# Kernel tuning notes

Hardware: AMD Instinct MI355X
Metric: run time of the kernel (lower is better)

Reference implementation:

```python
import jax, jax.numpy as jnp
import numpy as np

NUM_HEADS = 8
NUM_KV_HEADS = 4
HEAD_DIM = 256
HIDDEN = 2048
SEQ = 4096
CHUNK_START = 2048
CHUNK_END = 4096
SOFTCAP = 50.0
EPS = 1e-6
ROPE_THETA = 10000.0
NEG_INF = -1e9


def _rms_norm(x, w, eps=EPS):
    # Gemma RMSNorm: computed in fp32, scale is (1 + w)
    x32 = x.astype(jnp.float32)
    out = x32 * jax.lax.rsqrt(jnp.mean(x32 * x32, axis=-1, keepdims=True) + eps)
    return (out * (1.0 + w.astype(jnp.float32))).astype(x.dtype)


def _rotate_half(x):
    h = x.shape[-1] // 2
    return jnp.concatenate([-x[..., h:], x[..., :h]], axis=-1)


def _apply_rope(x, cos, sin):
    # x: [B, S, H, D]; cos/sin: [B, S, D] -> unsqueeze head dim
    cos = cos[:, :, None, :]
    sin = sin[:, :, None, :]
    return x * cos + _rotate_half(x) * sin


def setup_inputs() -> dict:
    key = jax.random.key(0)
    ks = jax.random.split(key, 8)
    hidden_states = jax.random.normal(ks[0], (1, SEQ, HIDDEN), dtype=jnp.float32)
    # real RoPE tables
    inv_freq = 1.0 / (ROPE_THETA ** (np.arange(0, HEAD_DIM, 2, dtype=np.float32) / HEAD_DIM))
    pos = np.arange(SEQ, dtype=np.float32)
    freqs = np.outer(pos, inv_freq)                      # [S, D/2]
    emb = np.concatenate([freqs, freqs], axis=-1)        # [S, D]
    cos = jnp.asarray(np.cos(emb))[None]                 # [1, S, D]
    sin = jnp.asarray(np.sin(emb))[None]
    # causal additive mask for the chunk: query i (abs pos start+i) attends keys j <= start+i
    q_pos = np.arange(CHUNK_START, CHUNK_END)[:, None]
    k_pos = np.arange(CHUNK_END)[None, :]
    attention_mask = jnp.asarray(np.where(k_pos <= q_pos, 0.0, NEG_INF).astype(np.float32))[None, None]
    s = 0.02
    wq = jax.random.normal(ks[1], (HIDDEN, NUM_HEADS * HEAD_DIM), dtype=jnp.float32) * s
    wk = jax.random.normal(ks[2], (HIDDEN, NUM_KV_HEADS * HEAD_DIM), dtype=jnp.float32) * s
    wv = jax.random.normal(ks[3], (HIDDEN, NUM_KV_HEADS * HEAD_DIM), dtype=jnp.float32) * s
    wo = jax.random.normal(ks[4], (NUM_HEADS * HEAD_DIM, HIDDEN), dtype=jnp.float32) * s
    q_norm_w = jnp.zeros((HEAD_DIM,), dtype=jnp.float32)
    k_norm_w = jnp.zeros((HEAD_DIM,), dtype=jnp.float32)
    v_norm_w = jnp.zeros((HEAD_DIM,), dtype=jnp.float32)
    return {
        'hidden_states': hidden_states, 'cos': cos, 'sin': sin,
        'attention_mask': attention_mask,
        'wq': wq, 'wk': wk, 'wv': wv, 'wo': wo,
        'q_norm_w': q_norm_w, 'k_norm_w': k_norm_w, 'v_norm_w': v_norm_w,
        'start': CHUNK_START, 'end': CHUNK_END,
    }


def reference(hidden_states, cos, sin, attention_mask, wq, wk, wv, wo,
              q_norm_w, k_norm_w, v_norm_w, start, end):
    B = hidden_states.shape[0]
    chunk = end - start
    scaling = HEAD_DIM ** -0.5

    # ---- queries from the chunk ----
    q = (hidden_states[:, start:end] @ wq).reshape(B, chunk, NUM_HEADS, HEAD_DIM)
    q = _rms_norm(q, q_norm_w)
    q = _apply_rope(q, cos[:, start:end], sin[:, start:end])
    q = q.transpose(0, 2, 1, 3)                         # [B, H, chunk, D]

    # ---- keys / values over [0, end) ----
    kv_h = hidden_states[:, :end]
    k = (kv_h @ wk).reshape(B, end, NUM_KV_HEADS, HEAD_DIM)
    k = _rms_norm(k, k_norm_w)
    k = _apply_rope(k, cos[:, :end], sin[:, :end]).transpose(0, 2, 1, 3)   # [B, KV, end, D]
    v = (kv_h @ wv).reshape(B, end, NUM_KV_HEADS, HEAD_DIM)
    v = _rms_norm(v, v_norm_w).transpose(0, 2, 1, 3)                        # [B, KV, end, D]

    # ---- GQA repeat_kv ----
    n_rep = NUM_HEADS // NUM_KV_HEADS
    k = jnp.repeat(k, n_rep, axis=1)                    # [B, H, end, D]
    v = jnp.repeat(v, n_rep, axis=1)

    # ---- eager attention with logit softcap ----
    logits = jnp.einsum('bhqd,bhkd->bhqk', q, k) * scaling
    logits = jnp.tanh(logits / SOFTCAP) * SOFTCAP
    logits = logits + attention_mask
    attn = jax.nn.softmax(logits.astype(jnp.float32), axis=-1).astype(q.dtype)
    out = jnp.einsum('bhqk,bhkd->bhqd', attn, v)
    out = out.transpose(0, 2, 1, 3).reshape(B, chunk, NUM_HEADS * HEAD_DIM)
    return out @ wo
```

## Files before the change

kernel.cpp:

```cpp
#include <hip/hip_runtime.h>

#define HID 2048
#define SEQL 4096
#define CHUNK 2048
#define NHEADS 8
#define NKVH 4
#define HDIM 256

typedef __bf16 bf16x4 __attribute__((ext_vector_type(4)));
typedef __bf16 bf16x8 __attribute__((ext_vector_type(8)));
typedef float f32x4 __attribute__((ext_vector_type(4)));
typedef _Float16 f16x4 __attribute__((ext_vector_type(4)));
typedef __attribute__((address_space(1))) unsigned int* as1_u32;
typedef __attribute__((address_space(3))) unsigned int* as3_u32;

__device__ __forceinline__ void load_lds16(const __bf16* g, __bf16* l) {
  __builtin_amdgcn_global_load_lds((as1_u32)g, (as3_u32)l, 16, 0, 0);
}

__global__ void cvt_bf16_kernel(const float* __restrict__ X, __bf16* __restrict__ Y) {
  int i = blockIdx.x * blockDim.x + threadIdx.x;
  const float4* xv = (const float4*)X;
  float4 v = xv[i];
  bf16x4 o;
  o[0] = (__bf16)v.x; o[1] = (__bf16)v.y; o[2] = (__bf16)v.z; o[3] = (__bf16)v.w;
  *(bf16x4*)(Y + i * 4) = o;
}

__global__ void transpose_all_kernel(const float* __restrict__ wq, const float* __restrict__ wk,
                                     const float* __restrict__ wv, const float* __restrict__ wo,
                                     __bf16* __restrict__ WQT, __bf16* __restrict__ WKVT,
                                     __bf16* __restrict__ WOT) {
  __shared__ float tile[64][65];
  const int b = blockIdx.x;
  const float* W;
  __bf16* WT;
  int R, C, bx, by;
  if (b < 1024) { W = wq; WT = WQT; R = 2048; C = 2048; bx = b & 31; by = b >> 5; }
  else if (b < 1536) { int q = b - 1024; W = wk; WT = WKVT; R = 2048; C = 1024; bx = q & 15; by = q >> 4; }
  else if (b < 2048) { int q = b - 1536; W = wv; WT = WKVT + (size_t)1024 * 2048; R = 2048; C = 1024; bx = q & 15; by = q >> 4; }
  else { int q = b - 2048; W = wo; WT = WOT; R = 2048; C = 2048; bx = q & 31; by = q >> 5; }
  int r0 = by * 64, c0 = bx * 64;
  for (int i = threadIdx.x; i < 4096; i += 256) {
    int r = i >> 6, c = i & 63;
    tile[r][c] = W[(size_t)(r0 + r) * C + c0 + c];
  }
  __syncthreads();
  for (int i = threadIdx.x; i < 4096; i += 256) {
    int c = i >> 6, r = i & 63;
    WT[(size_t)(c0 + c) * R + r0 + r] = (__bf16)tile[r][c];
  }
}

__global__ __launch_bounds__(256, 3) void proj_kernel(
    const __bf16* __restrict__ Xb, const __bf16* __restrict__ WQT,
    const __bf16* __restrict__ WKVT, __bf16* __restrict__ Qp, __bf16* __restrict__ KVp) {
  __shared__ __bf16 Asm[128 * 32];
  __shared__ __bf16 Bsm[128 * 32];
  const int tid = threadIdx.x;
  const int lane = tid & 63, wave = tid >> 6;
  const int quad = lane >> 4, l15 = lane & 15;
  const int b = blockIdx.x;
  const __bf16 *A, *B;
  __bf16* C;
  int m0, n0;
  if (b < 512) {
    A = Xb; B = WKVT; C = KVp;
    m0 = (b & 31) * 128; n0 = (b >> 5) * 128;
  } else {
    int q = b - 512;
    A = Xb + (size_t)2048 * 2048; B = WQT; C = Qp;
    m0 = (q & 15) * 128; n0 = (q >> 4) * 128;
  }
  const int wm = (wave & 1) * 64, wn = (wave >> 1) * 64;
  f32x4 acc[4][4];
#pragma unroll
  for (int i = 0; i < 4; i++)
#pragma unroll
    for (int j = 0; j < 4; j++) acc[i][j] = (f32x4){0.f, 0.f, 0.f, 0.f};

  const int rA = lane >> 2, cA = (lane & 3) * 8;

  for (int k0 = 0; k0 < 2048; k0 += 32) {
#pragma unroll
    for (int c = wave; c < 8; c += 4) {
      load_lds16(A + (size_t)(m0 + c * 16 + rA) * 2048 + k0 + cA, Asm + c * 512);
      load_lds16(B + (size_t)(n0 + c * 16 + rA) * 2048 + k0 + cA, Bsm + c * 512);
    }
    __syncthreads();
    bf16x8 af[4], bfr[4];
#pragma unroll
    for (int i = 0; i < 4; i++) {
      af[i] = *(const bf16x8*)(Asm + (wm + i * 16 + l15) * 32 + quad * 8);
      bfr[i] = *(const bf16x8*)(Bsm + (wn + i * 16 + l15) * 32 + quad * 8);
    }
#pragma unroll
    for (int mi = 0; mi < 4; mi++)
#pragma unroll
      for (int ni = 0; ni < 4; ni++)
        acc[mi][ni] = __builtin_amdgcn_mfma_f32_16x16x32_bf16(af[mi], bfr[ni], acc[mi][ni], 0, 0, 0);
    __syncthreads();
  }
#pragma unroll
  for (int mi = 0; mi < 4; mi++) {
    int r = m0 + wm + mi * 16 + quad * 4;
#pragma unroll
    for (int ni = 0; ni < 4; ni++) {
      int cc = n0 + wn + ni * 16 + l15;
#pragma unroll
      for (int j = 0; j < 4; j++)
        C[(size_t)(r + j) * 2048 + cc] = (__bf16)acc[mi][ni][j];
    }
  }
}

template <int NI, bool F32OUT>
__global__ __launch_bounds__(256, 2) void gemm_bt_kernel(
    const __bf16* __restrict__ A, const __bf16* __restrict__ B,
    void* __restrict__ Cv, int M, int N, int Kd) {
  constexpr int BN = NI * 32;
  __shared__ __bf16 Asm[128 * 32];
  __shared__ __bf16 Bsm[BN * 32];
  const int tid = threadIdx.x;
  const int lane = tid & 63, wave = tid >> 6;
  const int quad = lane >> 4, l15 = lane & 15;
  const int m0 = blockIdx.x * 128, n0 = blockIdx.y * BN;
  const int wm = (wave & 1) * 64, wn = (wave >> 1) * (NI * 16);
  f32x4 acc[4][NI];
#pragma unroll
  for (int i = 0; i < 4; i++)
#pragma unroll
    for (int j = 0; j < NI; j++) acc[i][j] = (f32x4){0.f, 0.f, 0.f, 0.f};

  const int rA = lane >> 2, cA = (lane & 3) * 8;

  for (int k0 = 0; k0 < Kd; k0 += 32) {
#pragma unroll
    for (int c = wave; c < 8; c += 4)
      load_lds16(A + (size_t)(m0 + c * 16 + rA) * Kd + k0 + cA, Asm + c * 512);
#pragma unroll
    for (int c = wave; c < BN / 16; c += 4)
      load_lds16(B + (size_t)(n0 + c * 16 + rA) * Kd + k0 + cA, Bsm + c * 512);
    __syncthreads();
    bf16x8 af[4], bfr[NI];
#pragma unroll
    for (int i = 0; i < 4; i++)
      af[i] = *(const bf16x8*)(Asm + (wm + i * 16 + l15) * 32 + quad * 8);
#pragma unroll
    for (int i = 0; i < NI; i++)
      bfr[i] = *(const bf16x8*)(Bsm + (wn + i * 16 + l15) * 32 + quad * 8);
#pragma unroll
    for (int mi = 0; mi < 4; mi++)
#pragma unroll
      for (int ni = 0; ni < NI; ni++)
        acc[mi][ni] = __builtin_amdgcn_mfma_f32_16x16x32_bf16(af[mi], bfr[ni], acc[mi][ni], 0, 0, 0);
    __syncthreads();
  }
#pragma unroll
  for (int mi = 0; mi < 4; mi++) {
    int r = m0 + wm + mi * 16 + quad * 4;
#pragma unroll
    for (int ni = 0; ni < NI; ni++) {
      int cc = n0 + wn + ni * 16 + l15;
#pragma unroll
      for (int j = 0; j < 4; j++) {
        if (F32OUT)
          ((float*)Cv)[(size_t)(r + j) * N + cc] = acc[mi][ni][j];
        else
          ((__bf16*)Cv)[(size_t)(r + j) * N + cc] = (__bf16)acc[mi][ni][j];
      }
    }
  }
}

__global__ void norm_all_kernel(__bf16* __restrict__ Qp, __bf16* __restrict__ KVp,
                                __bf16* __restrict__ VT,
                                const float* __restrict__ cosb, const float* __restrict__ sinb,
                                const float* __restrict__ qw, const float* __restrict__ kw,
                                const float* __restrict__ vw) {
  const int gw = (blockIdx.x * 256 + threadIdx.x) >> 6;
  const int lane = threadIdx.x & 63;
  const int d0 = lane * 4;

  __bf16* row;
  const float* w;
  int pos = -1;
  int vh = 0, vt = 0;
  bool isV = false;
  float prescale = 1.f;
  if (gw < 16384) {
    int t = gw >> 3, h = gw & 7;
    row = Qp + (size_t)t * 2048 + h * 256;
    w = qw; pos = t + 2048; prescale = 0.0625f;
  } else {
    int g2 = gw - 16384;
    int t = g2 >> 3, r = g2 & 7;
    if (r < 4) {
      row = KVp + (size_t)t * 2048 + r * 256;
      w = kw; pos = t;
    } else {
      row = KVp + (size_t)t * 2048 + 1024 + (r - 4) * 256;
      w = vw; isV = true; vh = r - 4; vt = t;
    }
  }

  bf16x4 rv = *(const bf16x4*)(row + d0);
  float x[4];
  float ss = 0.f;
#pragma unroll
  for (int j = 0; j < 4; j++) { x[j] = (float)rv[j]; ss += x[j] * x[j]; }
#pragma unroll
  for (int off = 1; off < 64; off <<= 1) ss += __shfl_xor(ss, off);
  float scale = rsqrtf(ss * (1.f / 256.f) + 1e-6f);
  float n[4];
#pragma unroll
  for (int j = 0; j < 4; j++) n[j] = x[j] * scale * (1.f + w[d0 + j]);

  if (!isV) {
    const float* cp = cosb + (size_t)pos * 256 + d0;
    const float* sp = sinb + (size_t)pos * 256 + d0;
    bf16x4 ov;
#pragma unroll
    for (int j = 0; j < 4; j++) {
      float other = __shfl_xor(n[j], 32);
      float rot = (lane < 32) ? -other : other;
      ov[j] = (__bf16)((n[j] * cp[j] + rot * sp[j]) * prescale);
    }
    *(bf16x4*)(row + d0) = ov;
  } else {
#pragma unroll
    for (int j = 0; j < 4; j++)
      VT[(size_t)vh * (256 * 4096) + (size_t)(d0 + j) * 4096 + vt] = (__bf16)n[j];
  }
}

__global__ __launch_bounds__(256, 2) void attn_kernel(
    const __bf16* __restrict__ Q,
    const __bf16* __restrict__ K,
    const __bf16* __restrict__ VT,
    _Float16* __restrict__ Op,
    float* __restrict__ Lp) {
  __shared__ __bf16 Ksm[2][8][32][32];
  __shared__ __bf16 Vsm[2][256][32];
  __shared__ __bf16 Pex[4][32][40];
  const int tid = threadIdx.x;
  const int lane = tid & 63, wave = tid >> 6;
  const int quad = lane >> 4, l15 = lane & 15;
  const int b = blockIdx.x;
  const int idx = b & 255;
  const int h = idx & 7, sp = (idx >> 3) & 3;
  int qt = idx >> 5;
  if (b >= 256) qt = 15 - qt;
  const int kvh = h >> 1;

  const int T = 68 + 4 * qt;
  const int nst = T >> 2;

  bf16x8 qf[2][8];
#pragma unroll
  for (int r = 0; r < 2; r++) {
    const __bf16* qp = Q + (size_t)(qt * 128 + wave * 32 + r * 16 + l15) * 2048 + h * 256 + quad * 8;
#pragma unroll
    for (int s = 0; s < 8; s++) qf[r][s] = *(const bf16x8*)(qp + s * 32);
  }
  f32x4 o[2][16];
#pragma unroll
  for (int r = 0; r < 2; r++)
#pragma unroll
    for (int i = 0; i < 16; i++) o[r][i] = (f32x4){0.f, 0.f, 0.f, 0.f};
  float rs[2][4] = {{0.f, 0.f, 0.f, 0.f}, {0.f, 0.f, 0.f, 0.f}};

  const __bf16* Kb = K + kvh * 256;
  const __bf16* Vb = VT + (size_t)kvh * (256 * 4096);
  const int rA = lane >> 2;
  const int cAs = (((lane & 3) ^ ((rA >> 1) & 3)) * 8);
  const int kx = (quad ^ ((l15 >> 1) & 3)) * 8;
  const int qbase = 2048 + qt * 128 + wave * 32 + quad * 4;

  {
    const int t0 = sp * 32;
#pragma unroll
    for (int ch = 0; ch < 4; ch++) {
      int cc = wave + ch * 4;
      int s = cc >> 1, hf = cc & 1;
      load_lds16(Kb + (size_t)(t0 + hf * 16 + rA) * 2048 + s * 32 + cAs, &Ksm[0][s][hf * 16][0]);
      load_lds16(Vb + (size_t)(cc * 16 + rA) * 4096 + t0 + cAs, &Vsm[0][cc * 16][0]);
    }
  }

  for (int i = 0; i < nst; i++) {
    const int buf = i & 1;
    const int t0 = (4 * i + sp) * 32;
    __syncthreads();
    if (i + 1 < nst) {
      const int t1 = t0 + 128;
#pragma unroll
      for (int ch = 0; ch < 4; ch++) {
        int cc = wave + ch * 4;
        int s = cc >> 1, hf = cc & 1;
        load_lds16(Kb + (size_t)(t1 + hf * 16 + rA) * 2048 + s * 32 + cAs, &Ksm[buf ^ 1][s][hf * 16][0]);
        load_lds16(Vb + (size_t)(cc * 16 + rA) * 4096 + t1 + cAs, &Vsm[buf ^ 1][cc * 16][0]);
      }
    }

    f32x4 s4[2][2];
    s4[0][0] = (f32x4){0.f, 0.f, 0.f, 0.f};
    s4[0][1] = s4[0][0]; s4[1][0] = s4[0][0]; s4[1][1] = s4[0][0];
    __builtin_amdgcn_s_setprio(1);
#pragma unroll
    for (int s = 0; s < 8; s++) {
      bf16x8 b0 = *(const bf16x8*)(&Ksm[buf][s][l15][kx]);
      bf16x8 b1 = *(const bf16x8*)(&Ksm[buf][s][16 + l15][kx]);
      s4[0][0] = __builtin_amdgcn_mfma_f32_16x16x32_bf16(qf[0][s], b0, s4[0][0], 0, 0, 0);
      s4[0][1] = __builtin_amdgcn_mfma_f32_16x16x32_bf16(qf[0][s], b1, s4[0][1], 0, 0, 0);
      s4[1][0] = __builtin_amdgcn_mfma_f32_16x16x32_bf16(qf[1][s], b0, s4[1][0], 0, 0, 0);
      s4[1][1] = __builtin_amdgcn_mfma_f32_16x16x32_bf16(qf[1][s], b1, s4[1][1], 0, 0, 0);
    }
    __builtin_amdgcn_s_setprio(0);

    const bool mk = (i == nst - 1);
#pragma unroll
    for (int r = 0; r < 2; r++)
#pragma unroll
      for (int nt = 0; nt < 2; nt++) {
        const int key = t0 + nt * 16 + l15;
#pragma unroll
        for (int j = 0; j < 4; j++) {
          float v = s4[r][nt][j];
          float e = __expf(v * 0.04f);
          float p = __expf(-100.f * __builtin_amdgcn_rcpf(e + 1.f));
          if (mk && key > qbase + r * 16 + j) p = 0.f;
          s4[r][nt][j] = p;
          rs[r][j] += p;
        }
      }

#pragma unroll
    for (int r = 0; r < 2; r++)
#pragma unroll
      for (int nt = 0; nt < 2; nt++)
#pragma unroll
        for (int j = 0; j < 4; j++)
          Pex[wave][r * 16 + quad * 4 + j][nt * 16 + l15] = (__bf16)s4[r][nt][j];

    bf16x8 pf0 = *(const bf16x8*)(&Pex[wave][l15][quad * 8]);
    bf16x8 pf1 = *(const bf16x8*)(&Pex[wave][16 + l15][quad * 8]);
    __builtin_amdgcn_s_setprio(1);
#pragma unroll
    for (int d = 0; d < 16; d++) {
      bf16x8 vf = *(const bf16x8*)(&Vsm[buf][d * 16 + l15][kx]);
      o[0][d] = __builtin_amdgcn_mfma_f32_16x16x32_bf16(pf0, vf, o[0][d], 0, 0, 0);
      o[1][d] = __builtin_amdgcn_mfma_f32_16x16x32_bf16(pf1, vf, o[1][d], 0, 0, 0);
    }
    __builtin_amdgcn_s_setprio(0);
  }

#pragma unroll
  for (int off = 1; off < 16; off <<= 1)
#pragma unroll
    for (int r = 0; r < 2; r++)
#pragma unroll
      for (int j = 0; j < 4; j++) rs[r][j] += __shfl_xor(rs[r][j], off);

  _Float16* Os = Op + (size_t)sp * (2048 * 2048);
  float* Ls = Lp + sp * (2048 * 8);
#pragma unroll
  for (int r = 0; r < 2; r++) {
    float inv[4];
#pragma unroll
    for (int j = 0; j < 4; j++)
      inv[j] = rs[r][j] > 0.f ? 1.f / rs[r][j] : 0.f;
    const int trow = qt * 128 + wave * 32 + r * 16 + quad * 4;
#pragma unroll
    for (int d = 0; d < 16; d++) {
      const int col = h * 256 + d * 16 + l15;
#pragma unroll
      for (int j = 0; j < 4; j++)
        Os[(size_t)(trow + j) * 2048 + col] = (_Float16)(o[r][d][j] * inv[j]);
    }
    if (l15 == 0) {
#pragma unroll
      for (int j = 0; j < 4; j++) Ls[(trow + j) * 8 + h] = rs[r][j];
    }
  }
}

__global__ void merge_kernel(const _Float16* __restrict__ Op, const float* __restrict__ Lp,
                             __bf16* __restrict__ AO) {
  int f = (blockIdx.x * 256 + threadIdx.x) * 4;
  int q = f >> 11, col = f & 2047, h = col >> 8;
  float lsum = 0.f;
  float acc[4] = {0.f, 0.f, 0.f, 0.f};
#pragma unroll
  for (int s = 0; s < 4; s++) {
    float l = Lp[s * (2048 * 8) + q * 8 + h];
    lsum += l;
    f16x4 v = *(const f16x4*)(Op + (size_t)s * (2048 * 2048) + f);
#pragma unroll
    for (int j = 0; j < 4; j++) acc[j] += l * (float)v[j];
  }
  float inv = 1.f / lsum;
  bf16x4 o;
#pragma unroll
  for (int j = 0; j < 4; j++) o[j] = (__bf16)(acc[j] * inv);
  *(bf16x4*)(AO + f) = o;
}

extern "C" void kernel_launch(void* const* d_in, const int* in_sizes, int n_in,
                              void* d_out, int out_size, void* d_ws, size_t ws_size,
                              hipStream_t stream) {
  const float* hidden = (const float*)d_in[0];
  const float* cosb = (const float*)d_in[1];
  const float* sinb = (const float*)d_in[2];
  const float* wq = (const float*)d_in[4];
  const float* wk = (const float*)d_in[5];
  const float* wv = (const float*)d_in[6];
  const float* wo = (const float*)d_in[7];
  const float* qw = (const float*)d_in[8];
  const float* kw = (const float*)d_in[9];
  const float* vw = (const float*)d_in[10];
  float* outp = (float*)d_out;

  char* p = (char*)d_ws;
  __bf16* Xb = (__bf16*)p;   p += (size_t)SEQL * HID * 2;
  __bf16* WQT = (__bf16*)p;  p += (size_t)2048 * 2048 * 2;
  __bf16* WKVT = (__bf16*)p; p += (size_t)2048 * 2048 * 2;
  __bf16* WOT = (__bf16*)p;  p += (size_t)2048 * 2048 * 2;
  __bf16* Qp = (__bf16*)p;   p += (size_t)2048 * 2048 * 2;
  __bf16* KVp = (__bf16*)p;  p += (size_t)4096 * 2048 * 2;
  __bf16* VT = (__bf16*)p;   p += (size_t)4 * 256 * 4096 * 2;
  __bf16* AO = (__bf16*)p;   p += (size_t)2048 * 2048 * 2;
  float* Lpart = (float*)p;  p += (size_t)4 * 2048 * 8 * 4;
  _Float16* Opart = (_Float16*)Xb;

  cvt_bf16_kernel<<<8192, 256, 0, stream>>>(hidden, Xb);
  transpose_all_kernel<<<3072, 256, 0, stream>>>(wq, wk, wv, wo, WQT, WKVT, WOT);

  proj_kernel<<<768, 256, 0, stream>>>(Xb, WQT, WKVT, Qp, KVp);

  norm_all_kernel<<<12288, 256, 0, stream>>>(Qp, KVp, VT, cosb, sinb, qw, kw, vw);

  attn_kernel<<<512, 256, 0, stream>>>(Qp, KVp, VT, Opart, Lpart);
  merge_kernel<<<4096, 256, 0, stream>>>(Opart, Lpart, AO);

  gemm_bt_kernel<2, true><<<dim3(16, 32), 256, 0, stream>>>(AO, WOT, outp, 2048, 2048, 2048);
}
```

Baseline: 401.1 us.

## Double-buffer LDS tiles in projection GEMMs and drop setprio in attention

The projection and generic GEMM kernels now keep two LDS buffers per operand. The next K-slice is prefetched with global_load_lds while MFMAs run on the current one, and only one barrier is used per iteration. This is meant to hide global-load latency behind compute, at the cost of doubled LDS use, which can reduce occupancy. The attention kernel also drops its s_setprio priority bumps around the MFMA loops.

New measurement: 389.1 us. 3.0% less time.

```diff
diff --git a/kernel.cpp b/kernel.cpp
--- a/kernel.cpp
+++ b/kernel.cpp
@@ -55,8 +55,8 @@
 __global__ __launch_bounds__(256, 3) void proj_kernel(
     const __bf16* __restrict__ Xb, const __bf16* __restrict__ WQT,
     const __bf16* __restrict__ WKVT, __bf16* __restrict__ Qp, __bf16* __restrict__ KVp) {
-  __shared__ __bf16 Asm[128 * 32];
-  __shared__ __bf16 Bsm[128 * 32];
+  __shared__ __bf16 Asm[2][128 * 32];
+  __shared__ __bf16 Bsm[2][128 * 32];
   const int tid = threadIdx.x;
   const int lane = tid & 63, wave = tid >> 6;
   const int quad = lane >> 4, l15 = lane & 15;
@@ -81,25 +81,33 @@
 
   const int rA = lane >> 2, cA = (lane & 3) * 8;
 
+#pragma unroll
+  for (int c = wave; c < 8; c += 4) {
+    load_lds16(A + (size_t)(m0 + c * 16 + rA) * 2048 + cA, &Asm[0][c * 512]);
+    load_lds16(B + (size_t)(n0 + c * 16 + rA) * 2048 + cA, &Bsm[0][c * 512]);
+  }
+
   for (int k0 = 0; k0 < 2048; k0 += 32) {
-#pragma unroll
-    for (int c = wave; c < 8; c += 4) {
-      load_lds16(A + (size_t)(m0 + c * 16 + rA) * 2048 + k0 + cA, Asm + c * 512);
-      load_lds16(B + (size_t)(n0 + c * 16 + rA) * 2048 + k0 + cA, Bsm + c * 512);
-    }
+    const int buf = (k0 >> 5) & 1;
     __syncthreads();
+    if (k0 + 32 < 2048) {
+#pragma unroll
+      for (int c = wave; c < 8; c += 4) {
+        load_lds16(A + (size_t)(m0 + c * 16 + rA) * 2048 + k0 + 32 + cA, &Asm[buf ^ 1][c * 512]);
+        load_lds16(B + (size_t)(n0 + c * 16 + rA) * 2048 + k0 + 32 + cA, &Bsm[buf ^ 1][c * 512]);
+      }
+    }
     bf16x8 af[4], bfr[4];
 #pragma unroll
     for (int i = 0; i < 4; i++) {
-      af[i] = *(const bf16x8*)(Asm + (wm + i * 16 + l15) * 32 + quad * 8);
-      bfr[i] = *(const bf16x8*)(Bsm + (wn + i * 16 + l15) * 32 + quad * 8);
+      af[i] = *(const bf16x8*)(&Asm[buf][(wm + i * 16 + l15) * 32 + quad * 8]);
+      bfr[i] = *(const bf16x8*)(&Bsm[buf][(wn + i * 16 + l15) * 32 + quad * 8]);
     }
 #pragma unroll
     for (int mi = 0; mi < 4; mi++)
 #pragma unroll
       for (int ni = 0; ni < 4; ni++)
         acc[mi][ni] = __builtin_amdgcn_mfma_f32_16x16x32_bf16(af[mi], bfr[ni], acc[mi][ni], 0, 0, 0);
-    __syncthreads();
   }
 #pragma unroll
   for (int mi = 0; mi < 4; mi++) {
@@ -119,8 +127,8 @@
     const __bf16* __restrict__ A, const __bf16* __restrict__ B,
     void* __restrict__ Cv, int M, int N, int Kd) {
   constexpr int BN = NI * 32;
-  __shared__ __bf16 Asm[128 * 32];
-  __shared__ __bf16 Bsm[BN * 32];
+  __shared__ __bf16 Asm[2][128 * 32];
+  __shared__ __bf16 Bsm[2][BN * 32];
   const int tid = threadIdx.x;
   const int lane = tid & 63, wave = tid >> 6;
   const int quad = lane >> 4, l15 = lane & 15;
@@ -134,27 +142,36 @@
 
   const int rA = lane >> 2, cA = (lane & 3) * 8;
 
+#pragma unroll
+  for (int c = wave; c < 8; c += 4)
+    load_lds16(A + (size_t)(m0 + c * 16 + rA) * Kd + cA, &Asm[0][c * 512]);
+#pragma unroll
+  for (int c = wave; c < BN / 16; c += 4)
+    load_lds16(B + (size_t)(n0 + c * 16 + rA) * Kd + cA, &Bsm[0][c * 512]);
+
   for (int k0 = 0; k0 < Kd; k0 += 32) {
-#pragma unroll
-    for (int c = wave; c < 8; c += 4)
-      load_lds16(A + (size_t)(m0 + c * 16 + rA) * Kd + k0 + cA, Asm + c * 512);
-#pragma unroll
-    for (int c = wave; c < BN / 16; c += 4)
-      load_lds16(B + (size_t)(n0 + c * 16 + rA) * Kd + k0 + cA, Bsm + c * 512);
+    const int buf = (k0 >> 5) & 1;
     __syncthreads();
+    if (k0 + 32 < Kd) {
+#pragma unroll
+      for (int c = wave; c < 8; c += 4)
+        load_lds16(A + (size_t)(m0 + c * 16 + rA) * Kd + k0 + 32 + cA, &Asm[buf ^ 1][c * 512]);
+#pragma unroll
+      for (int c = wave; c < BN / 16; c += 4)
+        load_lds16(B + (size_t)(n0 + c * 16 + rA) * Kd + k0 + 32 + cA, &Bsm[buf ^ 1][c * 512]);
+    }
     bf16x8 af[4], bfr[NI];
 #pragma unroll
     for (int i = 0; i < 4; i++)
-      af[i] = *(const bf16x8*)(Asm + (wm + i * 16 + l15) * 32 + quad * 8);
+      af[i] = *(const bf16x8*)(&Asm[buf][(wm + i * 16 + l15) * 32 + quad * 8]);
 #pragma unroll
     for (int i = 0; i < NI; i++)
-      bfr[i] = *(const bf16x8*)(Bsm + (wn + i * 16 + l15) * 32 + quad * 8);
+      bfr[i] = *(const bf16x8*)(&Bsm[buf][(wn + i * 16 + l15) * 32 + quad * 8]);
 #pragma unroll
     for (int mi = 0; mi < 4; mi++)
 #pragma unroll
       for (int ni = 0; ni < NI; ni++)
         acc[mi][ni] = __builtin_amdgcn_mfma_f32_16x16x32_bf16(af[mi], bfr[ni], acc[mi][ni], 0, 0, 0);
-    __syncthreads();
   }
 #pragma unroll
   for (int mi = 0; mi < 4; mi++) {
@@ -306,7 +323,6 @@
     f32x4 s4[2][2];
     s4[0][0] = (f32x4){0.f, 0.f, 0.f, 0.f};
     s4[0][1] = s4[0][0]; s4[1][0] = s4[0][0]; s4[1][1] = s4[0][0];
-    __builtin_amdgcn_s_setprio(1);
 #pragma unroll
     for (int s = 0; s < 8; s++) {
       bf16x8 b0 = *(const bf16x8*)(&Ksm[buf][s][l15][kx]);
@@ -316,7 +332,6 @@
       s4[1][0] = __builtin_amdgcn_mfma_f32_16x16x32_bf16(qf[1][s], b0, s4[1][0], 0, 0, 0);
       s4[1][1] = __builtin_amdgcn_mfma_f32_16x16x32_bf16(qf[1][s], b1, s4[1][1], 0, 0, 0);
     }
-    __builtin_amdgcn_s_setprio(0);
 
     const bool mk = (i == nst - 1);
 #pragma unroll
@@ -345,14 +360,12 @@
 
     bf16x8 pf0 = *(const bf16x8*)(&Pex[wave][l15][quad * 8]);
     bf16x8 pf1 = *(const bf16x8*)(&Pex[wave][16 + l15][quad * 8]);
-    __builtin_amdgcn_s_setprio(1);
 #pragma unroll
     for (int d = 0; d < 16; d++) {
       bf16x8 vf = *(const bf16x8*)(&Vsm[buf][d * 16 + l15][kx]);
       o[0][d] = __builtin_amdgcn_mfma_f32_16x16x32_bf16(pf0, vf, o[0][d], 0, 0, 0);
       o[1][d] = __builtin_amdgcn_mfma_f32_16x16x32_bf16(pf1, vf, o[1][d], 0, 0, 0);
     }
-    __builtin_amdgcn_s_setprio(0);
   }
 
 #pragma unroll
```
